# Performance work log

Measured on AMD Instinct MI355X. Metric: run time of the kernel, lower is better.

Reference implementation:

```python
import jax, jax.numpy as jnp
import numpy as np

NUM_USERS = 100000
NUM_ITEMS = 50000
N_NODES = NUM_USERS + NUM_ITEMS
NUM_COMMUNITY = 64
N_LAYERS = 3
NNZ = 2400000
BATCH = 8192
NEG_SLOPE = 0.1
EPS = 1e-12


def setup_inputs() -> dict:
    key = jax.random.key(0)
    ks = jax.random.split(key, 9)
    stdv = 1.0 / np.sqrt(NUM_COMMUNITY)
    return {
        "users": jax.random.randint(ks[0], (BATCH,), 0, NUM_USERS, dtype=jnp.int64 if jax.config.jax_enable_x64 else jnp.int32).astype(jnp.int32),
        "adjacent_items": jax.random.randint(ks[1], (BATCH,), 0, NUM_ITEMS).astype(jnp.int32),
        "weak_items": jax.random.randint(ks[2], (BATCH,), 0, NUM_ITEMS).astype(jnp.int32),
        "strong_items": jax.random.randint(ks[3], (BATCH,), 0, NUM_ITEMS).astype(jnp.int32),
        "edge_rows": jax.random.randint(ks[4], (NNZ,), 0, N_NODES).astype(jnp.int32),
        "edge_cols": jax.random.randint(ks[5], (NNZ,), 0, N_NODES).astype(jnp.int32),
        "edge_vals": jax.random.uniform(ks[6], (NNZ,), dtype=jnp.float32),
        "user_preference": jax.random.uniform(ks[7], (NUM_USERS, NUM_COMMUNITY), dtype=jnp.float32, minval=-stdv, maxval=stdv),
        "item_preference": jax.random.uniform(ks[8], (NUM_ITEMS, NUM_COMMUNITY), dtype=jnp.float32, minval=-stdv, maxval=stdv),
    }


def _lrelu_l2norm(x):
    # leaky_relu(neg_slope=0.1) then L2-normalize along last dim (torch F.normalize semantics)
    x = jnp.where(x >= 0, x, NEG_SLOPE * x)
    norm = jnp.sqrt(jnp.sum(x * x, axis=-1, keepdims=True))
    return x / jnp.maximum(norm, EPS)


def reference(users, adjacent_items, weak_items, strong_items,
              edge_rows, edge_cols, edge_vals,
              user_preference, item_preference):
    # ---- computer(): LightGCN-style propagation over sparse adjacency ----
    pref = _lrelu_l2norm(jnp.concatenate([user_preference, item_preference], axis=0))  # [N, C]
    acc = pref
    p = pref
    for _ in range(N_LAYERS):
        # sparse.mm(Graph, p): gather source rows, scale by edge values, scatter-add into dest rows
        msg = edge_vals[:, None] * p[edge_cols]                      # [nnz, C]
        p = jax.ops.segment_sum(msg, edge_rows, num_segments=N_NODES)  # [N, C]
        p = _lrelu_l2norm(p)
        acc = acc + p
    merged = acc / (N_LAYERS + 1)  # mean over stacked layers
    users_pref = merged[:NUM_USERS]
    items_pref = merged[NUM_USERS:]

    # ---- forward(): per-pair dot products + sigmoid ----
    u = users_pref[users]  # [B, C]

    def score(items):
        return jax.nn.sigmoid(jnp.sum(u * items_pref[items], axis=-1))

    # stack of (adjacent, weak, strong) gamma preferences, shape [3, B]
    return jnp.stack([score(adjacent_items), score(weak_items), score(strong_items)], axis=0)
```

## Files before the change

### kernel.cpp

```cpp
#include <hip/hip_runtime.h>
#include <hip/hip_fp16.h>
#include <math.h>

#define D 64
#define NUM_USERS 100000
#define NUM_ITEMS 50000
#define N_NODES 150000
#define NNZ 2400000
#define BATCH 8192
#define NEG_SLOPE 0.1f
#define EPS_NRM 1e-12f

#define NB2     293
#define RPB     512
#define NCHUNK  256
#define CH      9376
#define CAPB    9472
#define CAP     10240
#define VSCALE  16383.f

typedef unsigned short ushort_t;
typedef int   iv4 __attribute__((ext_vector_type(4)));
typedef float fv4 __attribute__((ext_vector_type(4)));

__device__ __forceinline__ float wave_sum64(float v) {
    #pragma unroll
    for (int off = 32; off > 0; off >>= 1)
        v += __shfl_xor(v, off, 64);
    return v;
}

__device__ __forceinline__ float h2f_lo(unsigned u) {
    return __half2float(__ushort_as_half((unsigned short)(u & 0xFFFFu)));
}
__device__ __forceinline__ float h2f_hi(unsigned u) {
    return __half2float(__ushort_as_half((unsigned short)(u >> 16)));
}

__global__ void __launch_bounds__(1024) scatter_init(
        const int* __restrict__ rows, const int* __restrict__ cols,
        const float* __restrict__ vals, int* __restrict__ gcur,
        uint2* __restrict__ es8,
        const float* __restrict__ upref, const float* __restrict__ ipref,
        __half* __restrict__ p0) {
    __shared__ int cnt[NB2];
    __shared__ int cur[NB2];
    int blk = blockIdx.x, tid = threadIdx.x;

    if (blk >= NCHUNK) {
        int row  = (blk - NCHUNK) * 16 + (tid >> 6);
        int lane = tid & 63;
        if (row >= N_NODES) return;
        float x = (row < NUM_USERS) ? upref[(size_t)row * D + lane]
                                    : ipref[(size_t)(row - NUM_USERS) * D + lane];
        x = (x >= 0.f) ? x : NEG_SLOPE * x;
        float norm = sqrtf(wave_sum64(x * x));
        float y = x / fmaxf(norm, EPS_NRM);
        p0[(size_t)row * D + lane] = __float2half(y);
        return;
    }

    for (int b = tid; b < NB2; b += 1024) cnt[b] = 0;
    __syncthreads();
    int base = blk * CH;
    int n = NNZ - base; if (n > CH) n = CH;
    const iv4* r4 = (const iv4*)(rows + base);
    for (int i = tid; i < (n >> 2); i += 1024) {
        iv4 r = r4[i];
        atomicAdd(&cnt[r.x >> 9], 1);
        atomicAdd(&cnt[r.y >> 9], 1);
        atomicAdd(&cnt[r.z >> 9], 1);
        atomicAdd(&cnt[r.w >> 9], 1);
    }
    __syncthreads();
    if (tid < NB2) {
        int c = cnt[tid];
        int off = (c > 0) ? atomicAdd(&gcur[tid], c) : 0;
        cur[tid] = tid * CAPB + off;
    }
    __syncthreads();
    const iv4* c4 = (const iv4*)(cols + base);
    const fv4* v4 = (const fv4*)(vals + base);
    for (int i = tid; i < (n >> 2); i += 1024) {
        iv4 r  = r4[i];
        iv4 cc = __builtin_nontemporal_load(&c4[i]);
        fv4 v  = __builtin_nontemporal_load(&v4[i]);
        int p;
        p = atomicAdd(&cur[r.x >> 9], 1);
        es8[p] = make_uint2((unsigned)cc.x | ((unsigned)(v.x * VSCALE + 0.5f) << 18),
                            (unsigned)(r.x & (RPB - 1)));
        p = atomicAdd(&cur[r.y >> 9], 1);
        es8[p] = make_uint2((unsigned)cc.y | ((unsigned)(v.y * VSCALE + 0.5f) << 18),
                            (unsigned)(r.y & (RPB - 1)));
        p = atomicAdd(&cur[r.z >> 9], 1);
        es8[p] = make_uint2((unsigned)cc.z | ((unsigned)(v.z * VSCALE + 0.5f) << 18),
                            (unsigned)(r.z & (RPB - 1)));
        p = atomicAdd(&cur[r.w >> 9], 1);
        es8[p] = make_uint2((unsigned)cc.w | ((unsigned)(v.w * VSCALE + 0.5f) << 18),
                            (unsigned)(r.w & (RPB - 1)));
    }
}

__global__ void __launch_bounds__(1024) bucket_sort(const uint2* __restrict__ es8,
                                                    const int* __restrict__ gcur,
                                                    unsigned* __restrict__ es,
                                                    int2* __restrict__ rowptr2) {
    __shared__ int      hist[RPB];
    __shared__ int      wsum[8];
    __shared__ unsigned outbuf[CAP];
    int b = blockIdx.x, tid = threadIdx.x;
    int base = b * CAPB;
    int fill = gcur[b];
    int end  = base + fill;
    if (tid < RPB) hist[tid] = 0;
    __syncthreads();
    for (int i = base + tid; i < end; i += 1024)
        atomicAdd(&hist[es8[i].y], 1);
    __syncthreads();
    int excl = 0, v = 0;
    if (tid < RPB) {
        v = hist[tid];
        int lane = tid & 63, w = tid >> 6;
        int s = v;
        #pragma unroll
        for (int off = 1; off < 64; off <<= 1) {
            int t = __shfl_up(s, off, 64);
            if (lane >= off) s += t;
        }
        if (lane == 63) wsum[w] = s;
        excl = s - v;
    }
    __syncthreads();
    if (tid == 0) {
        int a = 0;
        #pragma unroll
        for (int i = 0; i < 8; i++) { int t = wsum[i]; wsum[i] = a; a += t; }
    }
    __syncthreads();
    if (tid < RPB) {
        excl += wsum[tid >> 6];
        int r = b * RPB + tid;
        if (r < N_NODES)
            rowptr2[r] = make_int2(base + excl, base + excl + v);
        hist[tid] = excl;
    }
    __syncthreads();
    for (int i = base + tid; i < end; i += 1024) {
        uint2 kv = es8[i];
        int d = atomicAdd(&hist[kv.y], 1);
        outbuf[d] = kv.x;
    }
    __syncthreads();
    for (int i = tid; i < fill; i += 1024)
        es[base + i] = outbuf[i];
}

__device__ __forceinline__ void acc8(float a[8], float v, uint4 q) {
    a[0] = fmaf(v, h2f_lo(q.x), a[0]);
    a[1] = fmaf(v, h2f_hi(q.x), a[1]);
    a[2] = fmaf(v, h2f_lo(q.y), a[2]);
    a[3] = fmaf(v, h2f_hi(q.y), a[3]);
    a[4] = fmaf(v, h2f_lo(q.z), a[4]);
    a[5] = fmaf(v, h2f_hi(q.z), a[5]);
    a[6] = fmaf(v, h2f_lo(q.w), a[6]);
    a[7] = fmaf(v, h2f_hi(q.w), a[7]);
}

__global__ void gather_kernel(const int2* __restrict__ rowptr2,
                              const unsigned* __restrict__ es,
                              const __half* __restrict__ p,
                              __half* __restrict__ pn) {
    int tid  = threadIdx.x;
    int row  = blockIdx.x * 8 + (tid >> 5);
    if (row >= N_NODES) return;
    int hl   = tid & 31;
    int sub  = hl >> 3;
    int fl   = hl & 7;
    int2 rp  = rowptr2[row];
    int beg = rp.x, end = rp.y;

    float a[8];
    #pragma unroll
    for (int k = 0; k < 8; k++) a[k] = 0.f;

    const float vs = 1.f / VSCALE;
    int e = beg + sub;
    while (e + 4 < end) {
        unsigned ev0 = es[e];
        unsigned ev1 = es[e + 4];
        const uint4 q0 = *(const uint4*)(p + (((ev0 & 0x3FFFFu) << 6) | (fl << 3)));
        const uint4 q1 = *(const uint4*)(p + (((ev1 & 0x3FFFFu) << 6) | (fl << 3)));
        float v0 = (float)(ev0 >> 18) * vs;
        float v1 = (float)(ev1 >> 18) * vs;
        acc8(a, v0, q0);
        acc8(a, v1, q1);
        e += 8;
    }
    if (e < end) {
        unsigned ev = es[e];
        const uint4 q = *(const uint4*)(p + (((ev & 0x3FFFFu) << 6) | (fl << 3)));
        float v = (float)(ev >> 18) * vs;
        acc8(a, v, q);
    }

    bool s0 = (sub & 1) != 0, s1 = (sub & 2) != 0;
    float b1[4];
    #pragma unroll
    for (int j = 0; j < 4; j++) {
        int c4 = (j >> 1) * 4, bb = j & 1;
        float keep = s0 ? a[c4 + 2 + bb] : a[c4 + bb];
        float send = s0 ? a[c4 + bb]     : a[c4 + 2 + bb];
        b1[j] = keep + __shfl_xor(send, 8, 64);
    }
    float cf[2];
    #pragma unroll
    for (int bb = 0; bb < 2; bb++) {
        float keep = s1 ? b1[2 + bb] : b1[bb];
        float send = s1 ? b1[bb]     : b1[2 + bb];
        cf[bb] = keep + __shfl_xor(send, 16, 64);
    }
    float y0 = (cf[0] >= 0.f) ? cf[0] : NEG_SLOPE * cf[0];
    float y1 = (cf[1] >= 0.f) ? cf[1] : NEG_SLOPE * cf[1];
    float ss = fmaf(y0, y0, y1 * y1);
    ss += __shfl_xor(ss, 16, 64);
    ss += __shfl_xor(ss, 8, 64);
    ss += __shfl_xor(ss, 4, 64);
    ss += __shfl_xor(ss, 2, 64);
    ss += __shfl_xor(ss, 1, 64);
    float inv = 1.f / fmaxf(sqrtf(ss), EPS_NRM);
    __half2 o = __floats2half2_rn(y0 * inv, y1 * inv);
    *(__half2*)(pn + (size_t)row * D + fl * 8 + 2 * sub) = o;
}

__global__ void score_kernel(const int* __restrict__ users,
                             const int* __restrict__ it0,
                             const int* __restrict__ it1,
                             const int* __restrict__ it2,
                             const __half* __restrict__ p0,
                             const __half* __restrict__ p1,
                             const __half* __restrict__ p2,
                             const __half* __restrict__ p3,
                             float* __restrict__ out) {
    int b    = blockIdx.x * 4 + (threadIdx.x >> 6);
    int lane = threadIdx.x & 63;
    if (b >= BATCH) return;
    int u = users[b];
    size_t uo = (size_t)u * D + lane;
    float uf = __half2float(p0[uo]) + __half2float(p1[uo])
             + __half2float(p2[uo]) + __half2float(p3[uo]);

    int its[3];
    its[0] = it0[b]; its[1] = it1[b]; its[2] = it2[b];
    #pragma unroll
    for (int k = 0; k < 3; k++) {
        size_t io = (size_t)(NUM_USERS + its[k]) * D + lane;
        float itf = __half2float(p0[io]) + __half2float(p1[io])
                  + __half2float(p2[io]) + __half2float(p3[io]);
        float s = wave_sum64(uf * itf) * 0.0625f;
        if (lane == 0)
            out[k * BATCH + b] = 1.f / (1.f + expf(-s));
    }
}

extern "C" void kernel_launch(void* const* d_in, const int* in_sizes, int n_in,
                              void* d_out, int out_size, void* d_ws, size_t ws_size,
                              hipStream_t stream) {
    const int*   users  = (const int*)  d_in[0];
    const int*   adj    = (const int*)  d_in[1];
    const int*   weak   = (const int*)  d_in[2];
    const int*   strong = (const int*)  d_in[3];
    const int*   erows  = (const int*)  d_in[4];
    const int*   ecols  = (const int*)  d_in[5];
    const float* evals  = (const float*)d_in[6];
    const float* upref  = (const float*)d_in[7];
    const float* ipref  = (const float*)d_in[8];
    float* out = (float*)d_out;

    const size_t rowElems = (size_t)N_NODES * D;

    char* base = (char*)d_ws;
    size_t off = 0;
    auto alloc = [&](size_t bytes) {
        char* p = base + off;
        off = (off + bytes + 255) & ~(size_t)255;
        return (void*)p;
    };
    __half*   p0      = (__half*)  alloc(rowElems * sizeof(__half));
    __half*   p1      = (__half*)  alloc(rowElems * sizeof(__half));
    __half*   p2      = (__half*)  alloc(rowElems * sizeof(__half));
    __half*   p3      = (__half*)  alloc(rowElems * sizeof(__half));
    unsigned* es      = (unsigned*)alloc((size_t)NB2 * CAPB * 4);
    int2*     rowptr2 = (int2*)    alloc((size_t)N_NODES * sizeof(int2));
    int*      gcur    = (int*)     alloc(NB2 * sizeof(int));
    uint2*    es8t    = (uint2*)p2;

    hipMemsetAsync(gcur, 0, NB2 * sizeof(int), stream);
    scatter_init<<<NCHUNK + (N_NODES + 15) / 16, 1024, 0, stream>>>(
        erows, ecols, evals, gcur, es8t, upref, ipref, p0);
    bucket_sort<<<NB2, 1024, 0, stream>>>(es8t, gcur, es, rowptr2);

    gather_kernel<<<N_NODES / 8, 256, 0, stream>>>(rowptr2, es, p0, p1);
    gather_kernel<<<N_NODES / 8, 256, 0, stream>>>(rowptr2, es, p1, p2);
    gather_kernel<<<N_NODES / 8, 256, 0, stream>>>(rowptr2, es, p2, p3);

    score_kernel<<<(BATCH + 3) / 4, 256, 0, stream>>>(users, adj, weak, strong,
                                                      p0, p1, p2, p3, out);
}
```

Measured before the change: 321.0 us.

## Split each bucket_sort bucket into two half-row blocks for more parallelism

Each 512-row bucket is now sorted by two 512-thread blocks, one per 256-row half. Each block reads the whole bucket but keeps only edges of its half, then writes them to a fixed half-capacity region at offset HCAP. The aim is to double block count (586 vs 293) on a many-CU GPU and reduce LDS use per block so more blocks fit per CU. In exchange each block reads the bucket's input twice, and a half holding more than HCAP edges would overflow into the other half's output region.

```diff
diff --git a/kernel.cpp b/kernel.cpp
--- a/kernel.cpp
+++ b/kernel.cpp
@@ -16,7 +16,8 @@
 #define NCHUNK  256
 #define CH      9376
 #define CAPB    9472
-#define CAP     10240
+#define HCAP    4736
+#define CAPH    5120
 #define VSCALE  16383.f
 
 typedef unsigned short ushort_t;
@@ -101,24 +102,29 @@
     }
 }
 
-__global__ void __launch_bounds__(1024) bucket_sort(const uint2* __restrict__ es8,
-                                                    const int* __restrict__ gcur,
-                                                    unsigned* __restrict__ es,
-                                                    int2* __restrict__ rowptr2) {
-    __shared__ int      hist[RPB];
-    __shared__ int      wsum[8];
-    __shared__ unsigned outbuf[CAP];
-    int b = blockIdx.x, tid = threadIdx.x;
+__global__ void __launch_bounds__(512) bucket_sort(const uint2* __restrict__ es8,
+                                                   const int* __restrict__ gcur,
+                                                   unsigned* __restrict__ es,
+                                                   int2* __restrict__ rowptr2) {
+    __shared__ int      hist[256];
+    __shared__ int      wsum[4];
+    __shared__ unsigned outbuf[CAPH];
+    __shared__ int      sh_total;
+    int blk = blockIdx.x, tid = threadIdx.x;
+    int b = blk >> 1, h = blk & 1;
     int base = b * CAPB;
     int fill = gcur[b];
     int end  = base + fill;
-    if (tid < RPB) hist[tid] = 0;
-    __syncthreads();
-    for (int i = base + tid; i < end; i += 1024)
-        atomicAdd(&hist[es8[i].y], 1);
+    int obase = base + h * HCAP;
+    if (tid < 256) hist[tid] = 0;
+    __syncthreads();
+    for (int i = base + tid; i < end; i += 512) {
+        unsigned k = es8[i].y;
+        if ((int)(k >> 8) == h) atomicAdd(&hist[k & 255], 1);
+    }
     __syncthreads();
     int excl = 0, v = 0;
-    if (tid < RPB) {
+    if (tid < 256) {
         v = hist[tid];
         int lane = tid & 63, w = tid >> 6;
         int s = v;
@@ -134,25 +140,29 @@
     if (tid == 0) {
         int a = 0;
         #pragma unroll
-        for (int i = 0; i < 8; i++) { int t = wsum[i]; wsum[i] = a; a += t; }
-    }
-    __syncthreads();
-    if (tid < RPB) {
+        for (int i = 0; i < 4; i++) { int t = wsum[i]; wsum[i] = a; a += t; }
+    }
+    __syncthreads();
+    if (tid < 256) {
         excl += wsum[tid >> 6];
-        int r = b * RPB + tid;
+        int r = b * RPB + h * 256 + tid;
         if (r < N_NODES)
-            rowptr2[r] = make_int2(base + excl, base + excl + v);
+            rowptr2[r] = make_int2(obase + excl, obase + excl + v);
+        if (tid == 255) sh_total = excl + v;
         hist[tid] = excl;
     }
     __syncthreads();
-    for (int i = base + tid; i < end; i += 1024) {
+    for (int i = base + tid; i < end; i += 512) {
         uint2 kv = es8[i];
-        int d = atomicAdd(&hist[kv.y], 1);
-        outbuf[d] = kv.x;
-    }
-    __syncthreads();
-    for (int i = tid; i < fill; i += 1024)
-        es[base + i] = outbuf[i];
+        if ((int)(kv.y >> 8) == h) {
+            int d = atomicAdd(&hist[kv.y & 255], 1);
+            outbuf[d] = kv.x;
+        }
+    }
+    __syncthreads();
+    int total = sh_total;
+    for (int i = tid; i < total; i += 512)
+        es[obase + i] = outbuf[i];
 }
 
 __device__ __forceinline__ void acc8(float a[8], float v, uint4 q) {
@@ -297,7 +307,7 @@
     hipMemsetAsync(gcur, 0, NB2 * sizeof(int), stream);
     scatter_init<<<NCHUNK + (N_NODES + 15) / 16, 1024, 0, stream>>>(
         erows, ecols, evals, gcur, es8t, upref, ipref, p0);
-    bucket_sort<<<NB2, 1024, 0, stream>>>(es8t, gcur, es, rowptr2);
+    bucket_sort<<<NB2 * 2, 512, 0, stream>>>(es8t, gcur, es, rowptr2);
 
     gather_kernel<<<N_NODES / 8, 256, 0, stream>>>(rowptr2, es, p0, p1);
     gather_kernel<<<N_NODES / 8, 256, 0, stream>>>(rowptr2, es, p1, p2);
```

New measurement: 327.0 us. About the same (+1.9%).
